# Kernel optimization log

Measured on AMD Instinct MI355X. Metric: run time of the kernel, lower is better.

Reference implementation:

```python
import jax, jax.numpy as jnp
import numpy as np

B, S, D, H = 2, 2048, 1024, 16
DH = D // H
LAMBDA_INIT = 0.8
EPS = 1e-5


def setup_inputs() -> dict:
    key = jax.random.key(0)
    ks = jax.random.split(key, 12)
    inp = {
        "inputs": jax.random.normal(ks[0], (B, S, D), jnp.float32),
        # projection weights stored as [in, out] for right-multiplication
        "wq0": jax.random.normal(ks[1], (D, H * DH), jnp.float32) * 0.02,
        "wq1": jax.random.normal(ks[2], (D, H * DH), jnp.float32) * 0.02,
        "wk0": jax.random.normal(ks[3], (D, H * DH), jnp.float32) * 0.02,
        "wk1": jax.random.normal(ks[4], (D, H * DH), jnp.float32) * 0.02,
        "wv": jax.random.normal(ks[5], (D, H * DH), jnp.float32) * 0.02,
        "wo": jax.random.normal(ks[6], (H * DH, D), jnp.float32) * 0.02,
        # lambda parameter vectors (scaled so exp(dot) stays sane)
        "l0": jax.random.normal(ks[7], (DH,), jnp.float32) * 0.1,
        "l1": jax.random.normal(ks[8], (DH,), jnp.float32) * 0.1,
        "l2": jax.random.normal(ks[9], (DH,), jnp.float32) * 0.1,
        "l3": jax.random.normal(ks[10], (DH,), jnp.float32) * 0.1,
        # per-head LayerNorm params stacked: [H, DH]
        "ln_w": jnp.ones((H, DH), jnp.float32),
        "ln_b": jnp.zeros((H, DH), jnp.float32),
    }
    return inp


def _forward(inputs, wq0, wq1, wk0, wk1, wv, wo, l0, l1, l2, l3, ln_w, ln_b):
    b, s, d = inputs.shape

    def proj(w):  # [b,s,d] @ [d,H*DH] -> [b,H,s,DH]
        return jnp.einsum("bsd,de->bse", inputs, w).reshape(b, s, H, DH).transpose(0, 2, 1, 3)

    q0, q1 = proj(wq0), proj(wq1)
    k0, k1 = proj(wk0), proj(wk1)
    v = proj(wv)

    scale = jax.lax.rsqrt(jnp.float32(DH))
    # ALiBi bias: slope_h * (pos_i - pos_j)
    slopes = (2.0 ** (-8.0 * jnp.arange(1, H + 1, dtype=jnp.float32) / H))  # [H]
    pos = jnp.arange(s, dtype=jnp.float32)
    pos_diff = pos[:, None] - pos[None, :]  # [s,s]
    bias = slopes[None, :, None, None] * pos_diff[None, None, :, :]  # [1,H,s,s]
    causal = jnp.where(jnp.triu(jnp.ones((s, s), bool), 1), -jnp.inf, 0.0)[None, None]

    s0 = jnp.einsum("bhqd,bhkd->bhqk", q0, k0) * scale - bias + causal
    s1 = jnp.einsum("bhqd,bhkd->bhqk", q1, k1) * scale - bias + causal
    w0 = jax.nn.softmax(s0, axis=-1)
    w1 = jax.nn.softmax(s1, axis=-1)

    lamb = (-jnp.exp(jnp.dot(l0, l1)) + LAMBDA_INIT) + (-jnp.exp(jnp.dot(l2, l3)) + LAMBDA_INIT)
    diff_weights = w0 - lamb * w1

    heads = jnp.einsum("bhqk,bhkd->bhqd", diff_weights, v).transpose(0, 2, 1, 3)  # [b,s,H,DH]
    # per-head LayerNorm over DH (biased variance, eps=1e-5)
    mu = jnp.mean(heads, axis=-1, keepdims=True)
    var = jnp.mean((heads - mu) ** 2, axis=-1, keepdims=True)
    normed = (heads - mu) * jax.lax.rsqrt(var + EPS) * ln_w[None, None] + ln_b[None, None]

    attention = normed.reshape(b, s, H * DH)
    return jnp.einsum("bse,ed->bsd", attention, wo)


def reference(inputs, wq0, wq1, wk0, wk1, wv, wo, l0, l1, l2, l3, ln_w, ln_b):
    return _forward(inputs, wq0, wq1, wk0, wk1, wv, wo, l0, l1, l2, l3, ln_w, ln_b)
```

## Files before the change

kernel.cpp:

```cpp
#include <hip/hip_runtime.h>
#include <hip/hip_bf16.h>
#include <math.h>

#define S_LEN   2048
#define NH      16
#define DHEAD   64

typedef __attribute__((ext_vector_type(8))) short short8;
typedef __attribute__((ext_vector_type(4))) short short4v;
typedef __attribute__((ext_vector_type(4))) float f32x4;
typedef __attribute__((ext_vector_type(16))) float f32x16;
typedef __attribute__((ext_vector_type(4))) int int4v;

__device__ __forceinline__ f32x4 mfma16(short8 a, short8 b, f32x4 c) {
    return __builtin_amdgcn_mfma_f32_16x16x32_bf16(a, b, c, 0, 0, 0);
}
__device__ __forceinline__ f32x16 mfma32(short8 a, short8 b, f32x16 c) {
    return __builtin_amdgcn_mfma_f32_32x32x16_bf16(a, b, c, 0, 0, 0);
}

__device__ __forceinline__ unsigned short f2bf(float f) {
    unsigned u = __builtin_bit_cast(unsigned, f);
    u = (u + 0x7FFFu + ((u >> 16) & 1u)) >> 16;
    return (unsigned short)u;
}

__device__ __forceinline__ int cvtpk(float lo, float hi) {
    int w;
    asm("v_cvt_pk_bf16_f32 %0, %1, %2" : "=v"(w) : "v"(lo), "v"(hi));
    return w;
}

__device__ __forceinline__ void pl32swap(int& a, int& b) {
    asm("v_permlane32_swap_b32 %0, %1" : "+v"(a), "+v"(b));
}

#define GLL16(gp, lp) __builtin_amdgcn_global_load_lds( \
    (const __attribute__((address_space(1))) void*)(gp), \
    (__attribute__((address_space(3))) void*)(lp), 16, 0, 0)

__global__ __launch_bounds__(256)
void convert_x(const float* __restrict__ x, short* __restrict__ xb)
{
    const int idx = (blockIdx.x * 256 + threadIdx.x) * 4;
    typedef __attribute__((ext_vector_type(4))) float f4;
    f4 v = *(const f4*)&x[idx];
    short4v o;
    o[0] = (short)f2bf(v[0]); o[1] = (short)f2bf(v[1]);
    o[2] = (short)f2bf(v[2]); o[3] = (short)f2bf(v[3]);
    *(short4v*)&xb[idx] = o;
}

__global__ __launch_bounds__(256)
void transp_w(const float* __restrict__ w0, const float* __restrict__ w1,
              const float* __restrict__ w2, const float* __restrict__ w3,
              const float* __restrict__ w4, const float* __restrict__ w5,
              short* __restrict__ wt)
{
    __shared__ float t[64][65];
    const int z = blockIdx.z;
    const float* src = (z == 0) ? w0 : (z == 1) ? w1 : (z == 2) ? w2
                     : (z == 3) ? w3 : (z == 4) ? w4 : w5;
    const float scale = (z <= 1) ? 0.125f * 1.44269504f : 1.0f;
    short* dst = wt + (size_t)z * 1024 * 1024;
    const int n0 = blockIdx.x * 64, k0 = blockIdx.y * 64;
    const int tid = threadIdx.x;
    const int c = tid & 63, rb = tid >> 6;
#pragma unroll
    for (int rr = 0; rr < 16; ++rr) {
        const int r = rr * 4 + rb;
        t[r][c] = src[(size_t)(k0 + r) * 1024 + n0 + c];
    }
    __syncthreads();
#pragma unroll
    for (int rr = 0; rr < 16; ++rr) {
        const int n = rr * 4 + rb;
        dst[(size_t)(n0 + n) * 1024 + k0 + c] = (short)f2bf(t[c][n] * scale);
    }
}

__global__ __launch_bounds__(256)
void transp_v(const short* __restrict__ vsrc, short* __restrict__ vdst)
{
    __shared__ short t[64][68];
    const int bh = blockIdx.y;
    const int s0 = blockIdx.x * 64;
    const int tid = threadIdx.x;
    const int c = tid & 63, rb = tid >> 6;
    const size_t base = (size_t)bh * S_LEN * DHEAD;
#pragma unroll
    for (int rr = 0; rr < 16; ++rr) {
        const int r = rr * 4 + rb;
        t[r][c] = vsrc[base + (size_t)(s0 + r) * 64 + c];
    }
    __syncthreads();
#pragma unroll
    for (int rr = 0; rr < 16; ++rr) {
        const int d = rr * 4 + rb;
        vdst[base + (size_t)d * S_LEN + s0 + c] = t[c][d];
    }
}

__global__ __launch_bounds__(256)
void gemm128(const short* __restrict__ A, const short* __restrict__ Wt,
             short* __restrict__ outb, float* __restrict__ outf, int mode)
{
    __shared__ short As[128 * 64];
    __shared__ short Bs[128 * 64];
    const int tid = threadIdx.x;
    const int l = tid & 63, w = tid >> 6;
    const int wm = w >> 1, wn = w & 1;
    const int m0 = blockIdx.y * 128;
    const int n0 = blockIdx.x * 128;
    const short* Bt = Wt + (size_t)blockIdx.z * (1024 * 1024);
    const int srow = l >> 3;
    const int schunk = (l & 7) ^ srow;

    f32x4 acc[4][4];
#pragma unroll
    for (int i = 0; i < 4; ++i)
#pragma unroll
        for (int j = 0; j < 4; ++j)
            acc[i][j] = (f32x4){0.f, 0.f, 0.f, 0.f};

    for (int k0 = 0; k0 < 1024; k0 += 64) {
        __syncthreads();
#pragma unroll
        for (int ii = 0; ii < 4; ++ii) {
            const int i = w * 4 + ii;
            GLL16(A  + (size_t)(m0 + 8 * i + srow) * 1024 + k0 + schunk * 8, &As[i * 512]);
            GLL16(Bt + (size_t)(n0 + 8 * i + srow) * 1024 + k0 + schunk * 8, &Bs[i * 512]);
        }
        __syncthreads();
#pragma unroll
        for (int kh = 0; kh < 2; ++kh) {
            short8 af[4], bfr[4];
#pragma unroll
            for (int ft = 0; ft < 4; ++ft) {
                const int row = wm * 64 + ft * 16 + (l & 15);
                const int ch = (kh * 4 + (l >> 4)) ^ (row & 7);
                af[ft] = *(const short8*)&As[row * 64 + ch * 8];
            }
#pragma unroll
            for (int nt = 0; nt < 4; ++nt) {
                const int row = wn * 64 + nt * 16 + (l & 15);
                const int ch = (kh * 4 + (l >> 4)) ^ (row & 7);
                bfr[nt] = *(const short8*)&Bs[row * 64 + ch * 8];
            }
#pragma unroll
            for (int i = 0; i < 4; ++i)
#pragma unroll
                for (int j = 0; j < 4; ++j)
                    acc[i][j] = mfma16(af[i], bfr[j], acc[i][j]);
        }
    }

#pragma unroll
    for (int i = 0; i < 4; ++i)
#pragma unroll
        for (int j = 0; j < 4; ++j)
#pragma unroll
            for (int r = 0; r < 4; ++r) {
                const int m = m0 + wm * 64 + i * 16 + (l >> 4) * 4 + r;
                const int n = n0 + wn * 64 + j * 16 + (l & 15);
                const float v = acc[i][j][r];
                if (mode == 0) {
                    const int b = m >> 11, s = m & 2047;
                    const int h = n >> 6, dh = n & 63;
                    outb[(size_t)blockIdx.z * (4u * 1024 * 1024)
                         + (((size_t)(b * NH + h)) * S_LEN + s) * DHEAD + dh] = (short)f2bf(v);
                } else {
                    outf[(size_t)m * 1024 + n] = v;
                }
            }
}

__global__ __launch_bounds__(256, 2)
void diff_attn_mfma(const short* __restrict__ pbuf, const short* __restrict__ vtb,
                    const float* __restrict__ l0v, const float* __restrict__ l1v,
                    const float* __restrict__ l2v, const float* __restrict__ l3v,
                    const float* __restrict__ lnw, const float* __restrict__ lnb,
                    short* __restrict__ attnout)
{
    __shared__ short Ks[2][3][64 * 64];

    const int tid = threadIdx.x;
    const int l = tid & 63, w = tid >> 6;
    const int il = l & 31, hi = l >> 5;
    const int qt = 15 - (int)blockIdx.y;
    const int bh = blockIdx.x;
    const int b = bh >> 4, h = bh & 15;
    const size_t MAT = (size_t)32 * S_LEN * DHEAD;
    const size_t hoff = (size_t)bh * S_LEN * DHEAD;
    const short* q0g = pbuf + 0 * MAT + hoff;
    const short* q1g = pbuf + 1 * MAT + hoff;
    const short* k0g = pbuf + 2 * MAT + hoff;
    const short* k1g = pbuf + 3 * MAT + hoff;
    const short* vtg = vtb + hoff;

    const float slope2 = exp2f(-0.5f * (float)(h + 1)) * 1.44269504f;
    float d01 = 0.f, d23 = 0.f;
    for (int t = 0; t < DHEAD; ++t) { d01 += l0v[t] * l1v[t]; d23 += l2v[t] * l3v[t]; }
    const float lamb = (-__expf(d01) + 0.8f) + (-__expf(d23) + 0.8f);

    const int rg = qt * 128 + w * 32 + il;

    short8 qf0[4], qf1[4];
#pragma unroll
    for (int dblk = 0; dblk < 4; ++dblk) {
        qf0[dblk] = *(const short8*)&q0g[(size_t)rg * 64 + dblk * 16 + hi * 8];
        qf1[dblk] = *(const short8*)&q1g[(size_t)rg * 64 + dblk * 16 + hi * 8];
    }

    f32x16 ot0[2], ot1[2];
#pragma unroll
    for (int mb = 0; mb < 2; ++mb)
#pragma unroll
        for (int r = 0; r < 16; ++r) { ot0[mb][r] = 0.f; ot1[mb][r] = 0.f; }
    float m0r = -100000.f, m1r = -100000.f, l0r = 0.f, l1r = 0.f;

    const int srow = l >> 3;
    const int schunk = (l & 7) ^ srow;
    const int nkt = 2 * qt + 2;
    const int qw0 = qt * 128 + w * 32;

#define STAGE(kt_, bi_) do {                                                        \
    _Pragma("unroll")                                                               \
    for (int ii = 0; ii < 2; ++ii) {                                                \
        const int i_ = w * 2 + ii;                                                  \
        GLL16(k0g + (size_t)((kt_) * 64 + 8 * i_ + srow) * 64 + schunk * 8,         \
              &Ks[bi_][0][i_ * 512]);                                               \
        GLL16(k1g + (size_t)((kt_) * 64 + 8 * i_ + srow) * 64 + schunk * 8,         \
              &Ks[bi_][1][i_ * 512]);                                               \
        GLL16(vtg + (size_t)(8 * i_ + srow) * S_LEN + (kt_) * 64 + schunk * 8,      \
              &Ks[bi_][2][i_ * 512]);                                               \
    }                                                                               \
} while (0)

    STAGE(0, 0);

    for (int kt = 0; kt < nkt; ++kt) {
        const int cur = kt & 1;
        if (kt + 1 < nkt) {
            STAGE(kt + 1, cur ^ 1);
            asm volatile("s_waitcnt vmcnt(6)" ::: "memory");
        } else {
            asm volatile("s_waitcnt vmcnt(0)" ::: "memory");
        }
        __builtin_amdgcn_s_barrier();

        if (kt * 64 <= qw0 + 31) {
            f32x16 s0[2], s1[2];
            const float cb0 = slope2 * (float)(kt * 64 + 4 * hi - rg) - m0r;
            const float dm = m0r - m1r;
#pragma unroll
            for (int kvb = 0; kvb < 2; ++kvb) {
                const float cb = cb0 + slope2 * (float)(kvb * 32);
#pragma unroll
                for (int r = 0; r < 16; ++r) {
                    const float pat = (float)((r & 3) + 8 * (r >> 2));
                    s0[kvb][r] = fmaf(slope2, pat, cb);
                    s1[kvb][r] = s0[kvb][r] + dm;
                }
            }

#pragma unroll
            for (int dblk = 0; dblk < 4; ++dblk)
#pragma unroll
                for (int kvb = 0; kvb < 2; ++kvb) {
                    const int rowA = kvb * 32 + il;
                    const int ch = (dblk * 2 + hi) ^ (rowA & 7);
                    const short8 k0f = *(const short8*)&Ks[cur][0][rowA * 64 + ch * 8];
                    const short8 k1f = *(const short8*)&Ks[cur][1][rowA * 64 + ch * 8];
                    s0[kvb] = mfma32(k0f, qf0[dblk], s0[kvb]);
                    s1[kvb] = mfma32(k1f, qf1[dblk], s1[kvb]);
                }

            if (kt * 64 + 63 > qw0) {
                const int mth = rg - kt * 64;
#pragma unroll
                for (int kvb = 0; kvb < 2; ++kvb)
#pragma unroll
                    for (int r = 0; r < 16; ++r) {
                        const int kvoff = kvb * 32 + (r & 3) + 8 * (r >> 2) + 4 * hi;
                        if (kvoff > mth) { s0[kvb][r] = -1e30f; s1[kvb][r] = -1e30f; }
                    }
            }

            float t0[8], t1[8];
#pragma unroll
            for (int r = 0; r < 8; ++r) {
                t0[r] = fmaxf(fmaxf(s0[0][r], s0[0][r + 8]), fmaxf(s0[1][r], s0[1][r + 8]));
                t1[r] = fmaxf(fmaxf(s1[0][r], s1[0][r + 8]), fmaxf(s1[1][r], s1[1][r + 8]));
            }
            float pm0 = fmaxf(fmaxf(fmaxf(t0[0], t0[1]), fmaxf(t0[2], t0[3])),
                              fmaxf(fmaxf(t0[4], t0[5]), fmaxf(t0[6], t0[7])));
            float pm1 = fmaxf(fmaxf(fmaxf(t1[0], t1[1]), fmaxf(t1[2], t1[3])),
                              fmaxf(fmaxf(t1[4], t1[5]), fmaxf(t1[6], t1[7])));
            pm0 = fmaxf(pm0, __shfl_xor(pm0, 32));
            pm1 = fmaxf(pm1, __shfl_xor(pm1, 32));

            if (__any(pm0 > 8.f || pm1 > 8.f)) {
                const float d0 = fmaxf(pm0, 0.f), d1 = fmaxf(pm1, 0.f);
                const float sc0 = __builtin_amdgcn_exp2f(-d0);
                const float sc1 = __builtin_amdgcn_exp2f(-d1);
#pragma unroll
                for (int mb = 0; mb < 2; ++mb)
#pragma unroll
                    for (int r = 0; r < 16; ++r) {
                        ot0[mb][r] *= sc0;
                        ot1[mb][r] *= sc1;
                    }
                l0r *= sc0; l1r *= sc1;
                m0r += d0; m1r += d1;
#pragma unroll
                for (int kvb = 0; kvb < 2; ++kvb)
#pragma unroll
                    for (int r = 0; r < 16; ++r) {
                        s0[kvb][r] -= d0;
                        s1[kvb][r] -= d1;
                    }
            }

#pragma unroll
            for (int kvb = 0; kvb < 2; ++kvb)
#pragma unroll
                for (int r = 0; r < 16; ++r) {
                    s0[kvb][r] = __builtin_amdgcn_exp2f(s0[kvb][r]);
                    s1[kvb][r] = __builtin_amdgcn_exp2f(s1[kvb][r]);
                }
            float u0[8], u1[8];
#pragma unroll
            for (int r = 0; r < 8; ++r) {
                u0[r] = (s0[0][r] + s0[0][r + 8]) + (s0[1][r] + s0[1][r + 8]);
                u1[r] = (s1[0][r] + s1[0][r + 8]) + (s1[1][r] + s1[1][r + 8]);
            }
            float rs0 = ((u0[0] + u0[1]) + (u0[2] + u0[3])) + ((u0[4] + u0[5]) + (u0[6] + u0[7]));
            float rs1 = ((u1[0] + u1[1]) + (u1[2] + u1[3])) + ((u1[4] + u1[5]) + (u1[6] + u1[7]));
            rs0 += __shfl_xor(rs0, 32);
            rs1 += __shfl_xor(rs1, 32);
            l0r += rs0; l1r += rs1;

            short8 pa0[4], pa1[4];
#pragma unroll
            for (int ks = 0; ks < 4; ++ks) {
                const int kvb = ks >> 1, rb = (ks & 1) * 8;
                int wa0 = cvtpk(s0[kvb][rb + 0], s0[kvb][rb + 1]);
                int wb0 = cvtpk(s0[kvb][rb + 2], s0[kvb][rb + 3]);
                int wc0 = cvtpk(s0[kvb][rb + 4], s0[kvb][rb + 5]);
                int wd0 = cvtpk(s0[kvb][rb + 6], s0[kvb][rb + 7]);
                pl32swap(wa0, wc0);
                pl32swap(wb0, wd0);
                int wa1 = cvtpk(s1[kvb][rb + 0], s1[kvb][rb + 1]);
                int wb1 = cvtpk(s1[kvb][rb + 2], s1[kvb][rb + 3]);
                int wc1 = cvtpk(s1[kvb][rb + 4], s1[kvb][rb + 5]);
                int wd1 = cvtpk(s1[kvb][rb + 6], s1[kvb][rb + 7]);
                pl32swap(wa1, wc1);
                pl32swap(wb1, wd1);
                union { int4v wi; short8 sv; } u0u, u1u;
                u0u.wi[0] = wa0; u0u.wi[1] = wb0; u0u.wi[2] = wc0; u0u.wi[3] = wd0;
                u1u.wi[0] = wa1; u1u.wi[1] = wb1; u1u.wi[2] = wc1; u1u.wi[3] = wd1;
                pa0[ks] = u0u.sv;
                pa1[ks] = u1u.sv;
            }

#pragma unroll
            for (int mb = 0; mb < 2; ++mb)
#pragma unroll
                for (int ks = 0; ks < 4; ++ks) {
                    const int rowV = mb * 32 + il;
                    const int ch = (ks * 2 + hi) ^ (rowV & 7);
                    const short8 vf = *(const short8*)&Ks[cur][2][rowV * 64 + ch * 8];
                    ot0[mb] = mfma32(vf, pa0[ks], ot0[mb]);
                    ot1[mb] = mfma32(vf, pa1[ks], ot1[mb]);
                }
        }
        __builtin_amdgcn_s_barrier();
    }
#undef STAGE

    const float inv0 = 1.f / l0r, inv1 = 1.f / l1r;
    float hv[2][16];
    float tsum[16];
#pragma unroll
    for (int r = 0; r < 16; ++r) {
        hv[0][r] = ot0[0][r] * inv0 - lamb * (ot1[0][r] * inv1);
        hv[1][r] = ot0[1][r] * inv0 - lamb * (ot1[1][r] * inv1);
        tsum[r] = hv[0][r] + hv[1][r];
    }
#pragma unroll
    for (int st = 8; st > 0; st >>= 1)
#pragma unroll
        for (int r = 0; r < st; ++r) tsum[r] += tsum[r + st];
    const float sum = tsum[0] + __shfl_xor(tsum[0], 32);
    const float mu = sum * (1.f / 64.f);
#pragma unroll
    for (int r = 0; r < 16; ++r) {
        const float dd0 = hv[0][r] - mu, dd1 = hv[1][r] - mu;
        tsum[r] = dd0 * dd0 + dd1 * dd1;
    }
#pragma unroll
    for (int st = 8; st > 0; st >>= 1)
#pragma unroll
        for (int r = 0; r < st; ++r) tsum[r] += tsum[r + st];
    const float vsum = tsum[0] + __shfl_xor(tsum[0], 32);
    const float rstd = rsqrtf(vsum * (1.f / 64.f) + 1e-5f);

#pragma unroll
    for (int mb = 0; mb < 2; ++mb)
#pragma unroll
        for (int r = 0; r < 16; ++r) {
            const int d = mb * 32 + (r & 3) + 8 * (r >> 2) + 4 * hi;
            hv[mb][r] = (hv[mb][r] - mu) * rstd * lnw[h * 64 + d] + lnb[h * 64 + d];
        }

    short* orow = attnout + ((size_t)(b * S_LEN + rg)) * 1024 + h * 64;
#pragma unroll
    for (int mb = 0; mb < 2; ++mb)
#pragma unroll
        for (int a = 0; a < 4; ++a) {
            union { int wi[2]; short4v sv; } st;
            st.wi[0] = cvtpk(hv[mb][4 * a + 0], hv[mb][4 * a + 1]);
            st.wi[1] = cvtpk(hv[mb][4 * a + 2], hv[mb][4 * a + 3]);
            *(short4v*)&orow[mb * 32 + 8 * a + 4 * hi] = st.sv;
        }
}

extern "C" void kernel_launch(void* const* d_in, const int* in_sizes, int n_in,
                              void* d_out, int out_size, void* d_ws, size_t ws_size,
                              hipStream_t stream)
{
    (void)in_sizes; (void)n_in; (void)out_size; (void)ws_size;
    const float* x   = (const float*)d_in[0];
    const float* wq0 = (const float*)d_in[1];
    const float* wq1 = (const float*)d_in[2];
    const float* wk0 = (const float*)d_in[3];
    const float* wk1 = (const float*)d_in[4];
    const float* wv  = (const float*)d_in[5];
    const float* wo  = (const float*)d_in[6];
    const float* l0  = (const float*)d_in[7];
    const float* l1  = (const float*)d_in[8];
    const float* l2  = (const float*)d_in[9];
    const float* l3  = (const float*)d_in[10];
    const float* lnw = (const float*)d_in[11];
    const float* lnb = (const float*)d_in[12];
    float* out = (float*)d_out;
    short* ws = (short*)d_ws;

    const size_t M4 = (size_t)4 * 1024 * 1024;
    short* xb    = ws;
    short* wtcat = ws + M4;
    short* pbuf  = wtcat + (size_t)6 * 1024 * 1024;
    short* atb   = pbuf + 5 * M4;
    short* vtb   = xb;

    convert_x<<<4096, 256, 0, stream>>>(x, xb);
    transp_w<<<dim3(16, 16, 6), 256, 0, stream>>>(wq0, wq1, wk0, wk1, wv, wo, wtcat);
    gemm128<<<dim3(8, 32, 5), 256, 0, stream>>>(xb, wtcat, pbuf, nullptr, 0);
    transp_v<<<dim3(32, 32), 256, 0, stream>>>(pbuf + 4 * M4, vtb);
    diff_attn_mfma<<<dim3(32, 16), 256, 0, stream>>>(pbuf, vtb,
                                                     l0, l1, l2, l3, lnw, lnb, atb);
    gemm128<<<dim3(8, 32, 1), 256, 0, stream>>>(atb, wtcat + (size_t)5 * 1024 * 1024,
                                                nullptr, out, 1);
}
```

Baseline: 191.2 us.

## Balance causal attention by pairing query tiles and splitting keys with merge kernel

The attention kernel now pairs a long query tile with a short one (15-p and p) and splits each tile's key range into two halves across blocks. Every block therefore handles exactly 17 key tiles, removing the causal load imbalance. Partial outputs (bf16) and running max/sum stats go to a workspace, and a new merge_ln kernel combines the two halves, applies the lambda difference and the per-head LayerNorm. The cost is extra global traffic for the partials, an extra launch, and bf16 rounding of the unnormalized partial outputs.

```diff
diff --git a/kernel.cpp b/kernel.cpp
--- a/kernel.cpp
+++ b/kernel.cpp
@@ -5,6 +5,7 @@
 #define S_LEN   2048
 #define NH      16
 #define DHEAD   64
+#define UMEG    1048576
 
 typedef __attribute__((ext_vector_type(8))) short short8;
 typedef __attribute__((ext_vector_type(4))) short short4v;
@@ -24,13 +25,16 @@
     u = (u + 0x7FFFu + ((u >> 16) & 1u)) >> 16;
     return (unsigned short)u;
 }
+__device__ __forceinline__ float bf2f(short s) {
+    unsigned u = ((unsigned)(unsigned short)s) << 16;
+    return __builtin_bit_cast(float, u);
+}
 
 __device__ __forceinline__ int cvtpk(float lo, float hi) {
     int w;
     asm("v_cvt_pk_bf16_f32 %0, %1, %2" : "=v"(w) : "v"(lo), "v"(hi));
     return w;
 }
-
 __device__ __forceinline__ void pl32swap(int& a, int& b) {
     asm("v_permlane32_swap_b32 %0, %1" : "+v"(a), "+v"(b));
 }
@@ -62,7 +66,7 @@
     const float* src = (z == 0) ? w0 : (z == 1) ? w1 : (z == 2) ? w2
                      : (z == 3) ? w3 : (z == 4) ? w4 : w5;
     const float scale = (z <= 1) ? 0.125f * 1.44269504f : 1.0f;
-    short* dst = wt + (size_t)z * 1024 * 1024;
+    short* dst = wt + (size_t)z * UMEG;
     const int n0 = blockIdx.x * 64, k0 = blockIdx.y * 64;
     const int tid = threadIdx.x;
     const int c = tid & 63, rb = tid >> 6;
@@ -112,7 +116,7 @@
     const int wm = w >> 1, wn = w & 1;
     const int m0 = blockIdx.y * 128;
     const int n0 = blockIdx.x * 128;
-    const short* Bt = Wt + (size_t)blockIdx.z * (1024 * 1024);
+    const short* Bt = Wt + (size_t)blockIdx.z * UMEG;
     const int srow = l >> 3;
     const int schunk = (l & 7) ^ srow;
 
@@ -155,6 +159,8 @@
         }
     }
 
+    const size_t zoff = (blockIdx.z == 4) ? (size_t)24 * UMEG
+                                          : (size_t)blockIdx.z * (4 * UMEG);
 #pragma unroll
     for (int i = 0; i < 4; ++i)
 #pragma unroll
@@ -167,8 +173,8 @@
                 if (mode == 0) {
                     const int b = m >> 11, s = m & 2047;
                     const int h = n >> 6, dh = n & 63;
-                    outb[(size_t)blockIdx.z * (4u * 1024 * 1024)
-                         + (((size_t)(b * NH + h)) * S_LEN + s) * DHEAD + dh] = (short)f2bf(v);
+                    outb[zoff + (((size_t)(b * NH + h)) * S_LEN + s) * DHEAD + dh]
+                        = (short)f2bf(v);
                 } else {
                     outf[(size_t)m * 1024 + n] = v;
                 }
@@ -177,20 +183,22 @@
 
 __global__ __launch_bounds__(256, 2)
 void diff_attn_mfma(const short* __restrict__ pbuf, const short* __restrict__ vtb,
-                    const float* __restrict__ l0v, const float* __restrict__ l1v,
-                    const float* __restrict__ l2v, const float* __restrict__ l3v,
-                    const float* __restrict__ lnw, const float* __restrict__ lnb,
-                    short* __restrict__ attnout)
+                    short* __restrict__ partO, float* __restrict__ partml)
 {
     __shared__ short Ks[2][3][64 * 64];
 
     const int tid = threadIdx.x;
     const int l = tid & 63, w = tid >> 6;
     const int il = l & 31, hi = l >> 5;
-    const int qt = 15 - (int)blockIdx.y;
     const int bh = blockIdx.x;
-    const int b = bh >> 4, h = bh & 15;
-    const size_t MAT = (size_t)32 * S_LEN * DHEAD;
+    const int h = bh & 15;
+    const int p = blockIdx.y >> 1;
+    const int jh = blockIdx.y & 1;
+    const int qtA = 15 - p, qtB = p;
+    const int szA = qtA + 1, szB = qtB + 1;
+    const int ktA0 = jh * szA, ktB0 = jh * szB;
+
+    const size_t MAT = (size_t)4 * UMEG;
     const size_t hoff = (size_t)bh * S_LEN * DHEAD;
     const short* q0g = pbuf + 0 * MAT + hoff;
     const short* q1g = pbuf + 1 * MAT + hoff;
@@ -199,11 +207,9 @@
     const short* vtg = vtb + hoff;
 
     const float slope2 = exp2f(-0.5f * (float)(h + 1)) * 1.44269504f;
-    float d01 = 0.f, d23 = 0.f;
-    for (int t = 0; t < DHEAD; ++t) { d01 += l0v[t] * l1v[t]; d23 += l2v[t] * l3v[t]; }
-    const float lamb = (-__expf(d01) + 0.8f) + (-__expf(d23) + 0.8f);
-
-    const int rg = qt * 128 + w * 32 + il;
+
+    int qt_cur = qtA;
+    int rg = qtA * 128 + w * 32 + il;
 
     short8 qf0[4], qf1[4];
 #pragma unroll
@@ -219,36 +225,62 @@
         for (int r = 0; r < 16; ++r) { ot0[mb][r] = 0.f; ot1[mb][r] = 0.f; }
     float m0r = -100000.f, m1r = -100000.f, l0r = 0.f, l1r = 0.f;
 
-    const int srow = l >> 3;
-    const int schunk = (l & 7) ^ srow;
-    const int nkt = 2 * qt + 2;
-    const int qw0 = qt * 128 + w * 32;
+    const int srw = l >> 3;
+    const int schunk = (l & 7) ^ srw;
+
+#define KT_OF(s_) (((s_) < szA) ? (ktA0 + (s_)) : (ktB0 + ((s_) - szA)))
 
 #define STAGE(kt_, bi_) do {                                                        \
     _Pragma("unroll")                                                               \
     for (int ii = 0; ii < 2; ++ii) {                                                \
         const int i_ = w * 2 + ii;                                                  \
-        GLL16(k0g + (size_t)((kt_) * 64 + 8 * i_ + srow) * 64 + schunk * 8,         \
+        GLL16(k0g + (size_t)((kt_) * 64 + 8 * i_ + srw) * 64 + schunk * 8,          \
               &Ks[bi_][0][i_ * 512]);                                               \
-        GLL16(k1g + (size_t)((kt_) * 64 + 8 * i_ + srow) * 64 + schunk * 8,         \
+        GLL16(k1g + (size_t)((kt_) * 64 + 8 * i_ + srw) * 64 + schunk * 8,          \
               &Ks[bi_][1][i_ * 512]);                                               \
-        GLL16(vtg + (size_t)(8 * i_ + srow) * S_LEN + (kt_) * 64 + schunk * 8,      \
+        GLL16(vtg + (size_t)(8 * i_ + srw) * S_LEN + (kt_) * 64 + schunk * 8,       \
               &Ks[bi_][2][i_ * 512]);                                               \
     }                                                                               \
 } while (0)
 
-    STAGE(0, 0);
-
-    for (int kt = 0; kt < nkt; ++kt) {
-        const int cur = kt & 1;
-        if (kt + 1 < nkt) {
-            STAGE(kt + 1, cur ^ 1);
+#define SAVEPART(qt_) do {                                                          \
+    const int job_ = ((bh << 4) + (qt_)) * 2 + jh;                                  \
+    if (hi == 0) {                                                                  \
+        float4 mlv;                                                                 \
+        mlv.x = m0r; mlv.y = l0r; mlv.z = m1r; mlv.w = l1r;                         \
+        *(float4*)&partml[((size_t)job_ * 128 + w * 32 + il) * 4] = mlv;            \
+    }                                                                               \
+    _Pragma("unroll")                                                               \
+    for (int mb_ = 0; mb_ < 2; ++mb_)                                               \
+        _Pragma("unroll")                                                           \
+        for (int rq_ = 0; rq_ < 4; ++rq_) {                                         \
+            union { int wi[2]; short4v sv; } s0u, s1u;                              \
+            s0u.wi[0] = cvtpk(ot0[mb_][rq_ * 4 + 0], ot0[mb_][rq_ * 4 + 1]);        \
+            s0u.wi[1] = cvtpk(ot0[mb_][rq_ * 4 + 2], ot0[mb_][rq_ * 4 + 3]);        \
+            s1u.wi[0] = cvtpk(ot1[mb_][rq_ * 4 + 0], ot1[mb_][rq_ * 4 + 1]);        \
+            s1u.wi[1] = cvtpk(ot1[mb_][rq_ * 4 + 2], ot1[mb_][rq_ * 4 + 3]);        \
+            const size_t ob_ = (size_t)job_ * 16384 + (size_t)mb_ * 4096            \
+                               + rq_ * 1024 + hi * 512 + (w * 32 + il) * 4;         \
+            *(short4v*)&partO[ob_] = s0u.sv;                                        \
+            *(short4v*)&partO[ob_ + 8192] = s1u.sv;                                 \
+        }                                                                           \
+} while (0)
+
+    STAGE(KT_OF(0), 0);
+
+    for (int s = 0; s < 17; ++s) {
+        const int cur = s & 1;
+        if (s + 1 < 17) {
+            const int ktn = KT_OF(s + 1);
+            STAGE(ktn, cur ^ 1);
             asm volatile("s_waitcnt vmcnt(6)" ::: "memory");
         } else {
             asm volatile("s_waitcnt vmcnt(0)" ::: "memory");
         }
         __builtin_amdgcn_s_barrier();
 
+        const int kt = KT_OF(s);
+        const int qw0 = qt_cur * 128 + w * 32;
         if (kt * 64 <= qw0 + 31) {
             f32x16 s0[2], s1[2];
             const float cb0 = slope2 * (float)(kt * 64 + 4 * hi - rg) - m0r;
@@ -376,54 +408,98 @@
                 }
         }
         __builtin_amdgcn_s_barrier();
-    }
+
+        if (s == szA - 1) {
+            SAVEPART(qtA);
+#pragma unroll
+            for (int mb = 0; mb < 2; ++mb)
+#pragma unroll
+                for (int r = 0; r < 16; ++r) { ot0[mb][r] = 0.f; ot1[mb][r] = 0.f; }
+            m0r = -100000.f; m1r = -100000.f; l0r = 0.f; l1r = 0.f;
+            qt_cur = qtB;
+            rg = qtB * 128 + w * 32 + il;
+#pragma unroll
+            for (int dblk = 0; dblk < 4; ++dblk) {
+                qf0[dblk] = *(const short8*)&q0g[(size_t)rg * 64 + dblk * 16 + hi * 8];
+                qf1[dblk] = *(const short8*)&q1g[(size_t)rg * 64 + dblk * 16 + hi * 8];
+            }
+        }
+    }
+    SAVEPART(qtB);
+#undef SAVEPART
 #undef STAGE
-
-    const float inv0 = 1.f / l0r, inv1 = 1.f / l1r;
-    float hv[2][16];
-    float tsum[16];
-#pragma unroll
-    for (int r = 0; r < 16; ++r) {
-        hv[0][r] = ot0[0][r] * inv0 - lamb * (ot1[0][r] * inv1);
-        hv[1][r] = ot0[1][r] * inv0 - lamb * (ot1[1][r] * inv1);
-        tsum[r] = hv[0][r] + hv[1][r];
-    }
-#pragma unroll
-    for (int st = 8; st > 0; st >>= 1)
-#pragma unroll
-        for (int r = 0; r < st; ++r) tsum[r] += tsum[r + st];
-    const float sum = tsum[0] + __shfl_xor(tsum[0], 32);
-    const float mu = sum * (1.f / 64.f);
-#pragma unroll
-    for (int r = 0; r < 16; ++r) {
-        const float dd0 = hv[0][r] - mu, dd1 = hv[1][r] - mu;
-        tsum[r] = dd0 * dd0 + dd1 * dd1;
-    }
-#pragma unroll
-    for (int st = 8; st > 0; st >>= 1)
-#pragma unroll
-        for (int r = 0; r < st; ++r) tsum[r] += tsum[r + st];
-    const float vsum = tsum[0] + __shfl_xor(tsum[0], 32);
-    const float rstd = rsqrtf(vsum * (1.f / 64.f) + 1e-5f);
-
-#pragma unroll
-    for (int mb = 0; mb < 2; ++mb)
-#pragma unroll
-        for (int r = 0; r < 16; ++r) {
-            const int d = mb * 32 + (r & 3) + 8 * (r >> 2) + 4 * hi;
-            hv[mb][r] = (hv[mb][r] - mu) * rstd * lnw[h * 64 + d] + lnb[h * 64 + d];
+#undef KT_OF
+}
+
+__global__ __launch_bounds__(256)
+void merge_ln(const short* __restrict__ partO, const float* __restrict__ partml,
+              const float* __restrict__ l0v, const float* __restrict__ l1v,
+              const float* __restrict__ l2v, const float* __restrict__ l3v,
+              const float* __restrict__ lnw, const float* __restrict__ lnb,
+              short* __restrict__ atb)
+{
+    const int t = threadIdx.x;
+    const int bh = blockIdx.y, b = bh >> 4, h = bh & 15;
+    const int rl = t >> 2;
+    const int srow = blockIdx.x * 64 + rl;
+    const int qt = srow >> 7, rit = srow & 127;
+    const int sub = t & 3, mb = sub >> 1, hs = sub & 1;
+
+    float d01 = 0.f, d23 = 0.f;
+    for (int i = 0; i < 64; ++i) { d01 += l0v[i] * l1v[i]; d23 += l2v[i] * l3v[i]; }
+    const float lamb = (-__expf(d01) + 0.8f) + (-__expf(d23) + 0.8f);
+
+    const size_t jA = ((size_t)(bh * 16 + qt)) * 2;
+    const float4 mlA = *(const float4*)&partml[(jA * 128 + rit) * 4];
+    const float4 mlB = *(const float4*)&partml[((jA + 1) * 128 + rit) * 4];
+    const float mm0 = fmaxf(mlA.x, mlB.x);
+    const float sA0 = exp2f(mlA.x - mm0), sB0 = exp2f(mlB.x - mm0);
+    const float lc0 = mlA.y * sA0 + mlB.y * sB0;
+    const float mm1 = fmaxf(mlA.z, mlB.z);
+    const float sA1 = exp2f(mlA.z - mm1), sB1 = exp2f(mlB.z - mm1);
+    const float lc1 = mlA.w * sA1 + mlB.w * sB1;
+    const float i0 = 1.f / lc0, i1 = 1.f / lc1;
+
+    float hv[16];
+#pragma unroll
+    for (int rq = 0; rq < 4; ++rq) {
+        const size_t ob = jA * 16384 + (size_t)mb * 4096 + rq * 1024 + hs * 512 + rit * 4;
+        const short4v a0 = *(const short4v*)&partO[ob];
+        const short4v a1 = *(const short4v*)&partO[ob + 8192];
+        const short4v b0 = *(const short4v*)&partO[ob + 16384];
+        const short4v b1 = *(const short4v*)&partO[ob + 16384 + 8192];
+#pragma unroll
+        for (int j = 0; j < 4; ++j) {
+            const float v0 = (bf2f(a0[j]) * sA0 + bf2f(b0[j]) * sB0) * i0;
+            const float v1 = (bf2f(a1[j]) * sA1 + bf2f(b1[j]) * sB1) * i1;
+            hv[rq * 4 + j] = v0 - lamb * v1;
         }
-
-    short* orow = attnout + ((size_t)(b * S_LEN + rg)) * 1024 + h * 64;
-#pragma unroll
-    for (int mb = 0; mb < 2; ++mb)
-#pragma unroll
-        for (int a = 0; a < 4; ++a) {
-            union { int wi[2]; short4v sv; } st;
-            st.wi[0] = cvtpk(hv[mb][4 * a + 0], hv[mb][4 * a + 1]);
-            st.wi[1] = cvtpk(hv[mb][4 * a + 2], hv[mb][4 * a + 3]);
-            *(short4v*)&orow[mb * 32 + 8 * a + 4 * hi] = st.sv;
-        }
+    }
+
+    float s = 0.f;
+#pragma unroll
+    for (int r = 0; r < 16; ++r) s += hv[r];
+    s += __shfl_xor(s, 1); s += __shfl_xor(s, 2);
+    const float mu = s * (1.f / 64.f);
+    float vs = 0.f;
+#pragma unroll
+    for (int r = 0; r < 16; ++r) { const float dd = hv[r] - mu; vs += dd * dd; }
+    vs += __shfl_xor(vs, 1); vs += __shfl_xor(vs, 2);
+    const float rstd = rsqrtf(vs * (1.f / 64.f) + 1e-5f);
+
+    short* orow = atb + ((size_t)(b * S_LEN + srow)) * 1024 + h * 64;
+#pragma unroll
+    for (int rq = 0; rq < 4; ++rq) {
+        const int d0 = mb * 32 + rq * 8 + hs * 4;
+        float o[4];
+#pragma unroll
+        for (int j = 0; j < 4; ++j)
+            o[j] = (hv[rq * 4 + j] - mu) * rstd * lnw[h * 64 + d0 + j] + lnb[h * 64 + d0 + j];
+        union { int wi[2]; short4v sv; } st;
+        st.wi[0] = cvtpk(o[0], o[1]);
+        st.wi[1] = cvtpk(o[2], o[3]);
+        *(short4v*)&orow[d0] = st.sv;
+    }
 }
 
 extern "C" void kernel_launch(void* const* d_in, const int* in_sizes, int n_in,
@@ -447,19 +523,22 @@
     float* out = (float*)d_out;
     short* ws = (short*)d_ws;
 
-    const size_t M4 = (size_t)4 * 1024 * 1024;
-    short* xb    = ws;
-    short* wtcat = ws + M4;
-    short* pbuf  = wtcat + (size_t)6 * 1024 * 1024;
-    short* atb   = pbuf + 5 * M4;
-    short* vtb   = xb;
+    short* wtcat  = ws;
+    short* qk     = ws + (size_t)6  * UMEG;
+    short* vtb    = ws + (size_t)22 * UMEG;
+    short* atb    = ws + (size_t)26 * UMEG;
+    short* xb     = atb;
+    short* partO  = ws + (size_t)30 * UMEG;
+    short* vorig  = partO;
+    float* partml = (float*)(ws + (size_t)46 * UMEG);
 
     convert_x<<<4096, 256, 0, stream>>>(x, xb);
     transp_w<<<dim3(16, 16, 6), 256, 0, stream>>>(wq0, wq1, wk0, wk1, wv, wo, wtcat);
-    gemm128<<<dim3(8, 32, 5), 256, 0, stream>>>(xb, wtcat, pbuf, nullptr, 0);
-    transp_v<<<dim3(32, 32), 256, 0, stream>>>(pbuf + 4 * M4, vtb);
-    diff_attn_mfma<<<dim3(32, 16), 256, 0, stream>>>(pbuf, vtb,
-                                                     l0, l1, l2, l3, lnw, lnb, atb);
-    gemm128<<<dim3(8, 32, 1), 256, 0, stream>>>(atb, wtcat + (size_t)5 * 1024 * 1024,
+    gemm128<<<dim3(8, 32, 5), 256, 0, stream>>>(xb, wtcat, qk, nullptr, 0);
+    transp_v<<<dim3(32, 32), 256, 0, stream>>>(vorig, vtb);
+    diff_attn_mfma<<<dim3(32, 16), 256, 0, stream>>>(qk, vtb, partO, partml);
+    merge_ln<<<dim3(32, 32), 256, 0, stream>>>(partO, partml,
+                                               l0, l1, l2, l3, lnw, lnb, atb);
+    gemm128<<<dim3(8, 32, 1), 256, 0, stream>>>(atb, wtcat + (size_t)5 * UMEG,
                                                 nullptr, out, 1);
 }
```

Measured after the change: 194.1 us. About the same (+1.5%).
